# Kernel tuning notes

Measured on AMD Instinct MI355X. Metric: run time of the kernel, lower is better.

Reference implementation:

```python
import jax, jax.numpy as jnp
import numpy as np

M = 8192
A_N, A_K = 64, 64  # out_factors[0], in_factors[0]
B_N, B_K = 64, 64  # out_factors[1], in_factors[1]
K = A_K * B_K
N = A_N * B_N


def setup_inputs() -> dict:
    key = jax.random.key(0)
    kx, ka, kb, kbias = jax.random.split(key, 4)
    x = jax.random.normal(kx, (M, K), dtype=jnp.float32)
    A = jax.random.normal(ka, (A_N, A_K), dtype=jnp.float32) * (1.0 / np.sqrt(A_K))
    B = jax.random.normal(kb, (B_N, B_K), dtype=jnp.float32) * (1.0 / np.sqrt(B_K))
    bias = jax.random.normal(kbias, (N,), dtype=jnp.float32) * 0.01
    return {"x": x, "A": A, "B": B, "bias": bias}


def reference(x, A, B, bias):
    # Y = X @ (A kron B)^T + bias, computed without materializing A kron B.
    # Column index n of the kron weight decomposes as n = p*B_N + q with
    # (A kron B)[n, k] = A[p, k//B_K] * B[q, k%B_K].
    m, k = x.shape
    a_n, a_k = A.shape
    b_n, b_k = B.shape
    xr = x.reshape(m, a_k, b_k)                    # [M, A_K, B_K]
    y = jnp.einsum('mab,qb->maq', xr, B)           # contract B factor
    y = jnp.einsum('maq,pa->mpq', y, A)            # contract A factor
    return y.reshape(m, a_n * b_n) + bias[None, :]
```

## Files before the change

### kernel.cpp

```cpp
#include <hip/hip_runtime.h>

typedef __attribute__((ext_vector_type(8))) short short8v;
typedef __attribute__((ext_vector_type(4))) short short4v;
typedef __attribute__((ext_vector_type(4))) float float4v;

__device__ __forceinline__ short f2bf(float f) {
  __bf16 h = (__bf16)f;
  return __builtin_bit_cast(short, h);
}

__device__ __forceinline__ short8v cvt8(float4 a, float4 b) {
  short8v r;
  r[0] = f2bf(a.x); r[1] = f2bf(a.y); r[2] = f2bf(a.z); r[3] = f2bf(a.w);
  r[4] = f2bf(b.x); r[5] = f2bf(b.y); r[6] = f2bf(b.z); r[7] = f2bf(b.w);
  return r;
}

__device__ __forceinline__ void stage_weight(const float* __restrict__ src,
                                             short* __restrict__ dst, int tid) {
  const int r = tid >> 2;
  const int c0 = (tid & 3) << 4;
  const float* p = src + r * 64 + c0;
  float4 f0 = reinterpret_cast<const float4*>(p)[0];
  float4 f1 = reinterpret_cast<const float4*>(p)[1];
  float4 f2 = reinterpret_cast<const float4*>(p)[2];
  float4 f3 = reinterpret_cast<const float4*>(p)[3];
  short8v g0 = cvt8(f0, f1), g1 = cvt8(f2, f3);
  const int sw = (r & 7) << 3;
  *reinterpret_cast<short8v*>(&dst[r * 64 + ((c0)     ^ sw)]) = g0;
  *reinterpret_cast<short8v*>(&dst[r * 64 + ((c0 + 8) ^ sw)]) = g1;
}

__global__ __launch_bounds__(256, 4)
void kron64_kernel(const float* __restrict__ x, const float* __restrict__ A,
                   const float* __restrict__ B, const float* __restrict__ bias,
                   float* __restrict__ out) {
  __shared__ short bw[4096];
  __shared__ short aw[4096];
  __shared__ short y1[2][4096];

  const int tid = threadIdx.x;
  const int w = tid >> 6;
  const int lane = tid & 63;
  const int g = lane >> 4;
  const int c = lane & 15;
  const int swz = (c & 7) << 3;

  stage_weight(B, bw, tid);
  stage_weight(A, aw, tid);

  const int rs = w >> 1;
  const int half = w & 1;
  const int m = blockIdx.x * 2 + rs;
  const float* xm = x + (size_t)m * 4096;
  short* yw = y1[rs];
  const float4v vzero = {0.f, 0.f, 0.f, 0.f};

  const int A0 = 2 * half;
  float4 xb[8];
  {
    const float* base = xm + (16 * A0 + c) * 64 + 8 * g;
#pragma unroll
    for (int atl = 0; atl < 2; ++atl)
#pragma unroll
      for (int kk = 0; kk < 2; ++kk) {
        const float* p = base + atl * 1024 + kk * 32;
        xb[(atl * 2 + kk) * 2 + 0] = reinterpret_cast<const float4*>(p)[0];
        xb[(atl * 2 + kk) * 2 + 1] = reinterpret_cast<const float4*>(p)[1];
      }
  }

  __syncthreads();

#pragma unroll
  for (int atl = 0; atl < 2; ++atl) {
    const int at = A0 + atl;
    float4v acc[4];
#pragma unroll
    for (int qt = 0; qt < 4; ++qt) acc[qt] = vzero;
#pragma unroll
    for (int kk = 0; kk < 2; ++kk) {
      short8v xf = cvt8(xb[(atl * 2 + kk) * 2], xb[(atl * 2 + kk) * 2 + 1]);
#pragma unroll
      for (int qt = 0; qt < 4; ++qt) {
        short8v bfrk = *reinterpret_cast<const short8v*>(
            &bw[(16 * qt + c) * 64 + ((32 * kk + 8 * g) ^ swz)]);
        acc[qt] = __builtin_amdgcn_mfma_f32_16x16x32_bf16(
            xf, bfrk, acc[qt], 0, 0, 0);
      }
    }
#pragma unroll
    for (int qt = 0; qt < 4; ++qt) {
      short4v v;
      v[0] = f2bf(acc[qt][0]); v[1] = f2bf(acc[qt][1]);
      v[2] = f2bf(acc[qt][2]); v[3] = f2bf(acc[qt][3]);
      int idx = ((16 * qt + c) * 64 + 16 * at + 4 * g) ^ swz;
      *reinterpret_cast<short4v*>(&yw[idx]) = v;
    }
  }

  __syncthreads();

  {
    short8v yfr[2][2];
#pragma unroll
    for (int qtl = 0; qtl < 2; ++qtl)
#pragma unroll
      for (int kk = 0; kk < 2; ++kk) {
        int idx = ((16 * (2 * half + qtl) + c) * 64) + ((32 * kk + 8 * g) ^ swz);
        yfr[qtl][kk] = *reinterpret_cast<const short8v*>(&yw[idx]);
      }

    float* om = out + (size_t)m * 4096;
#pragma unroll
    for (int pt = 0; pt < 4; ++pt) {
      short8v afr[2];
#pragma unroll
      for (int kk = 0; kk < 2; ++kk)
        afr[kk] = *reinterpret_cast<const short8v*>(
            &aw[(16 * pt + c) * 64 + ((32 * kk + 8 * g) ^ swz)]);
#pragma unroll
      for (int qtl = 0; qtl < 2; ++qtl) {
        const int n = (16 * pt + c) * 64 + 16 * (2 * half + qtl) + 4 * g;
        float4 bv = *reinterpret_cast<const float4*>(bias + n);
        float4v acc; acc[0] = bv.x; acc[1] = bv.y; acc[2] = bv.z; acc[3] = bv.w;
#pragma unroll
        for (int kk = 0; kk < 2; ++kk)
          acc = __builtin_amdgcn_mfma_f32_16x16x32_bf16(
              yfr[qtl][kk], afr[kk], acc, 0, 0, 0);
        *reinterpret_cast<float4v*>(om + n) = acc;
      }
    }
  }
}

extern "C" void kernel_launch(void* const* d_in, const int* in_sizes, int n_in,
                              void* d_out, int out_size, void* d_ws, size_t ws_size,
                              hipStream_t stream) {
  (void)in_sizes; (void)n_in; (void)out_size; (void)d_ws; (void)ws_size;
  const float* x    = (const float*)d_in[0];
  const float* A    = (const float*)d_in[1];
  const float* B    = (const float*)d_in[2];
  const float* bias = (const float*)d_in[3];
  float* out = (float*)d_out;

  dim3 grid(4096), block(256);
  hipLaunchKernelGGL(kron64_kernel, grid, block, 0, stream, x, A, B, bias, out);
}
```

Baseline: 55.45 us.

## Process four row-pairs per block with register double-buffered x prefetch

Each block now handles eight rows (four generations of two rows) instead of two. This amortises the A/B weight staging into LDS across more rows. While the current generation is being computed, the next generation's x loads are issued into a second register buffer. Full __syncthreads are replaced by an LDS-only waitcnt plus s_barrier so the outstanding global loads are not drained. The cost is more registers (occupancy hint lowered from 4 to 2) and a grid shrunk to 1024 blocks, which reduces parallelism.

```diff
diff --git a/kernel.cpp b/kernel.cpp
--- a/kernel.cpp
+++ b/kernel.cpp
@@ -31,7 +31,9 @@
   *reinterpret_cast<short8v*>(&dst[r * 64 + ((c0 + 8) ^ sw)]) = g1;
 }
 
-__global__ __launch_bounds__(256, 4)
+constexpr int GENS = 4;
+
+__global__ __launch_bounds__(256, 2)
 void kron64_kernel(const float* __restrict__ x, const float* __restrict__ A,
                    const float* __restrict__ B, const float* __restrict__ bias,
                    float* __restrict__ out) {
@@ -46,91 +48,109 @@
   const int c = lane & 15;
   const int swz = (c & 7) << 3;
 
+  const int rs = w >> 1;
+  const int half = w & 1;
+  const int A0 = 2 * half;
+  const int mbase = blockIdx.x * (2 * GENS);
+  short* yw = y1[rs];
+  const float4v vzero = {0.f, 0.f, 0.f, 0.f};
+
   stage_weight(B, bw, tid);
   stage_weight(A, aw, tid);
 
-  const int rs = w >> 1;
-  const int half = w & 1;
-  const int m = blockIdx.x * 2 + rs;
-  const float* xm = x + (size_t)m * 4096;
-  short* yw = y1[rs];
-  const float4v vzero = {0.f, 0.f, 0.f, 0.f};
+  float4 xb0[8], xb1[8];
 
-  const int A0 = 2 * half;
-  float4 xb[8];
-  {
-    const float* base = xm + (16 * A0 + c) * 64 + 8 * g;
+  auto issue = [&](float4* buf, int m) {
+    const float* base = x + (size_t)m * 4096 + (16 * A0 + c) * 64 + 8 * g;
 #pragma unroll
     for (int atl = 0; atl < 2; ++atl)
 #pragma unroll
       for (int kk = 0; kk < 2; ++kk) {
         const float* p = base + atl * 1024 + kk * 32;
-        xb[(atl * 2 + kk) * 2 + 0] = reinterpret_cast<const float4*>(p)[0];
-        xb[(atl * 2 + kk) * 2 + 1] = reinterpret_cast<const float4*>(p)[1];
+        buf[(atl * 2 + kk) * 2 + 0] = reinterpret_cast<const float4*>(p)[0];
+        buf[(atl * 2 + kk) * 2 + 1] = reinterpret_cast<const float4*>(p)[1];
       }
-  }
+  };
 
-  __syncthreads();
+  auto lgkm_barrier = [&]() {
+    __asm__ volatile("s_waitcnt lgkmcnt(0)" ::: "memory");
+    __builtin_amdgcn_s_barrier();
+    __asm__ volatile("" ::: "memory");
+  };
+
+  issue(xb0, mbase + rs);
+  lgkm_barrier();
 
 #pragma unroll
-  for (int atl = 0; atl < 2; ++atl) {
-    const int at = A0 + atl;
-    float4v acc[4];
+  for (int gen = 0; gen < GENS; ++gen) {
+    const int m = mbase + 2 * gen + rs;
+    float4* cur = (gen & 1) ? xb1 : xb0;
+    float4* nxt = (gen & 1) ? xb0 : xb1;
+
 #pragma unroll
-    for (int qt = 0; qt < 4; ++qt) acc[qt] = vzero;
+    for (int atl = 0; atl < 2; ++atl) {
+      const int at = A0 + atl;
+      float4v acc[4];
 #pragma unroll
-    for (int kk = 0; kk < 2; ++kk) {
-      short8v xf = cvt8(xb[(atl * 2 + kk) * 2], xb[(atl * 2 + kk) * 2 + 1]);
+      for (int qt = 0; qt < 4; ++qt) acc[qt] = vzero;
+#pragma unroll
+      for (int kk = 0; kk < 2; ++kk) {
+        short8v xf = cvt8(cur[(atl * 2 + kk) * 2], cur[(atl * 2 + kk) * 2 + 1]);
+#pragma unroll
+        for (int qt = 0; qt < 4; ++qt) {
+          short8v bfrk = *reinterpret_cast<const short8v*>(
+              &bw[(16 * qt + c) * 64 + ((32 * kk + 8 * g) ^ swz)]);
+          acc[qt] = __builtin_amdgcn_mfma_f32_16x16x32_bf16(
+              xf, bfrk, acc[qt], 0, 0, 0);
+        }
+      }
 #pragma unroll
       for (int qt = 0; qt < 4; ++qt) {
-        short8v bfrk = *reinterpret_cast<const short8v*>(
-            &bw[(16 * qt + c) * 64 + ((32 * kk + 8 * g) ^ swz)]);
-        acc[qt] = __builtin_amdgcn_mfma_f32_16x16x32_bf16(
-            xf, bfrk, acc[qt], 0, 0, 0);
+        short4v v;
+        v[0] = f2bf(acc[qt][0]); v[1] = f2bf(acc[qt][1]);
+        v[2] = f2bf(acc[qt][2]); v[3] = f2bf(acc[qt][3]);
+        int idx = ((16 * qt + c) * 64 + 16 * at + 4 * g) ^ swz;
+        *reinterpret_cast<short4v*>(&yw[idx]) = v;
       }
     }
+
+    if (gen + 1 < GENS) issue(nxt, m + 2);
+
+    lgkm_barrier();
+
+    {
+      short8v yfr[2][2];
 #pragma unroll
-    for (int qt = 0; qt < 4; ++qt) {
-      short4v v;
-      v[0] = f2bf(acc[qt][0]); v[1] = f2bf(acc[qt][1]);
-      v[2] = f2bf(acc[qt][2]); v[3] = f2bf(acc[qt][3]);
-      int idx = ((16 * qt + c) * 64 + 16 * at + 4 * g) ^ swz;
-      *reinterpret_cast<short4v*>(&yw[idx]) = v;
-    }
-  }
+      for (int qtl = 0; qtl < 2; ++qtl)
+#pragma unroll
+        for (int kk = 0; kk < 2; ++kk) {
+          int idx = ((16 * (2 * half + qtl) + c) * 64) + ((32 * kk + 8 * g) ^ swz);
+          yfr[qtl][kk] = *reinterpret_cast<const short8v*>(&yw[idx]);
+        }
 
-  __syncthreads();
-
-  {
-    short8v yfr[2][2];
+      float* om = out + (size_t)m * 4096;
 #pragma unroll
-    for (int qtl = 0; qtl < 2; ++qtl)
-#pragma unroll
-      for (int kk = 0; kk < 2; ++kk) {
-        int idx = ((16 * (2 * half + qtl) + c) * 64) + ((32 * kk + 8 * g) ^ swz);
-        yfr[qtl][kk] = *reinterpret_cast<const short8v*>(&yw[idx]);
-      }
-
-    float* om = out + (size_t)m * 4096;
-#pragma unroll
-    for (int pt = 0; pt < 4; ++pt) {
-      short8v afr[2];
-#pragma unroll
-      for (int kk = 0; kk < 2; ++kk)
-        afr[kk] = *reinterpret_cast<const short8v*>(
-            &aw[(16 * pt + c) * 64 + ((32 * kk + 8 * g) ^ swz)]);
-#pragma unroll
-      for (int qtl = 0; qtl < 2; ++qtl) {
-        const int n = (16 * pt + c) * 64 + 16 * (2 * half + qtl) + 4 * g;
-        float4 bv = *reinterpret_cast<const float4*>(bias + n);
-        float4v acc; acc[0] = bv.x; acc[1] = bv.y; acc[2] = bv.z; acc[3] = bv.w;
+      for (int pt = 0; pt < 4; ++pt) {
+        short8v afr[2];
 #pragma unroll
         for (int kk = 0; kk < 2; ++kk)
-          acc = __builtin_amdgcn_mfma_f32_16x16x32_bf16(
-              yfr[qtl][kk], afr[kk], acc, 0, 0, 0);
-        *reinterpret_cast<float4v*>(om + n) = acc;
+          afr[kk] = *reinterpret_cast<const short8v*>(
+              &aw[(16 * pt + c) * 64 + ((32 * kk + 8 * g) ^ swz)]);
+#pragma unroll
+        for (int qtl = 0; qtl < 2; ++qtl) {
+          const int n = (16 * pt + c) * 64 + 16 * (2 * half + qtl) + 4 * g;
+          float4 bv = *reinterpret_cast<const float4*>(bias + n);
+          float4v acc; acc[0] = bv.x; acc[1] = bv.y; acc[2] = bv.z; acc[3] = bv.w;
+#pragma unroll
+          for (int kk = 0; kk < 2; ++kk)
+            acc = __builtin_amdgcn_mfma_f32_16x16x32_bf16(
+                yfr[qtl][kk], afr[kk], acc, 0, 0, 0);
+          *reinterpret_cast<float4v*>(om + n) = acc;
+        }
       }
     }
+
+    if (gen + 1 < GENS) lgkm_barrier();
   }
 }
 
@@ -144,6 +164,6 @@
   const float* bias = (const float*)d_in[3];
   float* out = (float*)d_out;
 
-  dim3 grid(4096), block(256);
+  dim3 grid(8192 / (2 * GENS)), block(256);
   hipLaunchKernelGGL(kron64_kernel, grid, block, 0, stream, x, A, B, bias, out);
 }
```

New measurement: 55.48 us. Within noise of the previous version (+0.0%).
